# Kernel optimization log

Measured on AMD Instinct MI355X. Metric: run time of the kernel, lower is better.

The kernel has to match this reference:

```python
import jax, jax.numpy as jnp
import numpy as np

N_BOOK = 16  # == len_code; C() loop is only consistent when len_code == n_book


def setup_inputs() -> dict:
    key = jax.random.key(0)
    k1, k2 = jax.random.split(key)
    N = 32768
    D = 256        # len_code * n_book = 16 * 16
    n_classes = 4096
    features = jax.random.normal(k1, (N, D), dtype=jnp.float32)
    # Prototypes passed transposed relative to storage: [len_code*n_book, n_classes]
    Prototypes = jax.random.normal(k2, (D, n_classes), dtype=jnp.float32)
    return {"features": features, "Prototypes": Prototypes}


def reference(features, Prototypes):
    # Faithful to GPQSoftMaxNet.C: per-book matmul, concat over books, mean.
    # features: [N, len_code*n_book] split along dim 1 into chunks of width n_book
    # Prototypes: [len_code*n_book, n_classes] split along dim 0 into chunks of height n_book
    n_book = N_BOOK
    N, D = features.shape
    n_classes = Prototypes.shape[1]
    f = features.reshape(N, -1, n_book)          # [N, n_book(=len_code), n_book]
    P = Prototypes.reshape(-1, n_book, n_classes)  # [n_book(=len_code), n_book, n_classes]
    # mean over books of per-book GEMMs, fused into one einsum (no [N,C,n_book] intermediate)
    logits = jnp.einsum('nbd,bdc->nc', f, P) / jnp.float32(n_book)
    return logits
```

## Files before the change

### kernel.cpp

```cpp
#include <hip/hip_runtime.h>
#include <hip/hip_bf16.h>

typedef __attribute__((ext_vector_type(8))) short short8;
typedef __attribute__((ext_vector_type(4))) float f32x4;

static constexpr int MT = 32768;
static constexpr int KT = 256;
static constexpr int CT = 4096;

__device__ __forceinline__ unsigned short f2b(float f) {
  unsigned int b = __float_as_uint(f);
  b += 0x7FFFu + ((b >> 16) & 1u);
  return (unsigned short)(b >> 16);
}

__global__ void __launch_bounds__(256) cvt_kernel(const float* __restrict__ A,
                                                  const float* __restrict__ B,
                                                  unsigned short* __restrict__ Abf,
                                                  unsigned short* __restrict__ Bt) {
  __shared__ unsigned short tile[32][33];
  int bid = blockIdx.x, tid = threadIdx.x;
  if (bid < 4096) {
    int i = bid * 256 + tid;
    const float4 v0 = reinterpret_cast<const float4*>(A)[2 * i];
    const float4 v1 = reinterpret_cast<const float4*>(A)[2 * i + 1];
    short8 o;
    o[0] = (short)f2b(v0.x); o[1] = (short)f2b(v0.y);
    o[2] = (short)f2b(v0.z); o[3] = (short)f2b(v0.w);
    o[4] = (short)f2b(v1.x); o[5] = (short)f2b(v1.y);
    o[6] = (short)f2b(v1.z); o[7] = (short)f2b(v1.w);
    reinterpret_cast<short8*>(Abf)[i] = o;
  } else {
    int b = bid - 4096;
    int c0 = (b & 127) * 32, k0 = (b >> 7) * 32;
    int tx = tid & 31, ty0 = tid >> 5;
#pragma unroll
    for (int i = 0; i < 4; ++i) {
      int ty = ty0 + i * 8;
      tile[ty][tx] = f2b(B[(size_t)(k0 + ty) * CT + c0 + tx]);
    }
    __syncthreads();
#pragma unroll
    for (int i = 0; i < 4; ++i) {
      int cy = ty0 + i * 8;
      Bt[(size_t)(c0 + cy) * KT + k0 + tx] = tile[tx][cy];
    }
  }
}

__device__ __forceinline__ void gload16(const void* g, void* l) {
  __builtin_amdgcn_global_load_lds(
      (const __attribute__((address_space(1))) void*)g,
      (__attribute__((address_space(3))) void*)l, 16, 0, 0);
}

__global__ void __launch_bounds__(256, 2) gemm_kernel(const unsigned short* __restrict__ Abf,
                                                      const unsigned short* __restrict__ Btw,
                                                      float* __restrict__ O) {
  constexpr int BK = 32;
  __shared__ __align__(16) char smem[32 * 264 * 4];
  unsigned short* Al = (unsigned short*)smem;
  unsigned short* Bl = (unsigned short*)(smem + 8192);
  float* eb = (float*)smem;

  int bid = blockIdx.x;
  int wg = (bid & 7) * 512 + (bid >> 3);
  int tc = wg & 15;
  int tr = wg >> 4;
  int r0 = tr * 128, c0 = tc * 256;

  int tid = threadIdx.x;
  int lane = tid & 63, wid = tid >> 6;
  int wr = wid >> 1, wc = wid & 1;
  int l15 = lane & 15, l4 = lane >> 4;

  f32x4 acc[8][4] = {};

  for (int t = 0; t < KT / BK; ++t) {
    if (t) __syncthreads();
#pragma unroll
    for (int i = 0; i < 2; ++i) {
      int c = wid * 64 + i * 256 + lane;
      gload16(Abf + (size_t)(r0 + (c >> 2)) * KT + t * BK + (c & 3) * 8,
              Al + (wid * 64 + i * 256) * 8);
    }
#pragma unroll
    for (int i = 0; i < 4; ++i) {
      int c = wid * 64 + i * 256 + lane;
      gload16(Btw + (size_t)(c0 + (c >> 2)) * KT + t * BK + (c & 3) * 8,
              Bl + (wid * 64 + i * 256) * 8);
    }
    __syncthreads();

    short8 af[4], bf[8];
#pragma unroll
    for (int m = 0; m < 4; ++m)
      af[m] = *reinterpret_cast<const short8*>(Al + (wr * 64 + m * 16 + l15) * BK + l4 * 8);
#pragma unroll
    for (int n = 0; n < 8; ++n)
      bf[n] = *reinterpret_cast<const short8*>(Bl + (wc * 128 + n * 16 + l15) * BK + l4 * 8);
#pragma unroll
    for (int n = 0; n < 8; ++n)
#pragma unroll
      for (int m = 0; m < 4; ++m)
        acc[n][m] = __builtin_amdgcn_mfma_f32_16x16x32_bf16(bf[n], af[m], acc[n][m], 0, 0, 0);
  }

  const float s = 1.0f / 16.0f;
#pragma unroll
  for (int p = 0; p < 4; ++p) {
    __syncthreads();
    if (wr == (p >> 1)) {
#pragma unroll
      for (int mm = 0; mm < 2; ++mm) {
        int m = (p & 1) * 2 + mm;
#pragma unroll
        for (int n = 0; n < 8; ++n) {
          f32x4 v = acc[n][m];
          v[0] *= s; v[1] *= s; v[2] *= s; v[3] *= s;
          *reinterpret_cast<f32x4*>(
              &eb[(mm * 16 + l15) * 264 + wc * 128 + n * 16 + l4 * 4]) = v;
        }
      }
    }
    __syncthreads();
#pragma unroll
    for (int i = 0; i < 8; ++i) {
      int r = i * 4 + wid;
      f32x4 v = *reinterpret_cast<const f32x4*>(&eb[r * 264 + lane * 4]);
      __builtin_nontemporal_store(v, reinterpret_cast<f32x4*>(
          O + (size_t)(r0 + p * 32 + r) * CT + c0 + lane * 4));
    }
  }
}

__global__ void __launch_bounds__(256) naive_kernel(const float* __restrict__ A,
                                                    const float* __restrict__ B,
                                                    float* __restrict__ O) {
  size_t i = (size_t)blockIdx.x * 256 + threadIdx.x;
  int col = (int)(i & (size_t)(CT - 1));
  int row = (int)(i >> 12);
  float s = 0.f;
  for (int k = 0; k < KT; ++k)
    s += A[(size_t)row * KT + k] * B[(size_t)k * CT + col];
  O[i] = s * (1.0f / 16.0f);
}

extern "C" void kernel_launch(void* const* d_in, const int* in_sizes, int n_in,
                              void* d_out, int out_size, void* d_ws, size_t ws_size,
                              hipStream_t stream) {
  const float* A = (const float*)d_in[0];
  const float* B = (const float*)d_in[1];
  float* O = (float*)d_out;
  const size_t needA = (size_t)MT * KT * sizeof(unsigned short);
  const size_t needB = (size_t)CT * KT * sizeof(unsigned short);
  if (ws_size >= needA + needB) {
    unsigned short* Abf = (unsigned short*)d_ws;
    unsigned short* Btw = (unsigned short*)((char*)d_ws + needA);
    cvt_kernel<<<4096 + 1024, 256, 0, stream>>>(A, B, Abf, Btw);
    gemm_kernel<<<(MT / 128) * (CT / 256), 256, 0, stream>>>(Abf, Btw, O);
  } else {
    naive_kernel<<<(unsigned)((size_t)MT * CT / 256), 256, 0, stream>>>(A, B, O);
  }
}
```

Baseline: 135.9 us.

## Double GEMM K-tile to 64 and XOR-swizzle LDS layout

Raises the K tile from 32 to 64, halving the number of K iterations and their block-wide barriers. Each tile is consumed in two sub-steps of 32. The LDS layout is XOR-swizzled on the 16-byte slot index so that the longer 128-byte rows do not produce bank conflicts on the fragment reads. LDS use grows to 48 KB per block, which may limit how many blocks fit per CU alongside the launch bound of 2.

```diff
diff --git a/kernel.cpp b/kernel.cpp
--- a/kernel.cpp
+++ b/kernel.cpp
@@ -57,10 +57,10 @@
 __global__ void __launch_bounds__(256, 2) gemm_kernel(const unsigned short* __restrict__ Abf,
                                                       const unsigned short* __restrict__ Btw,
                                                       float* __restrict__ O) {
-  constexpr int BK = 32;
-  __shared__ __align__(16) char smem[32 * 264 * 4];
+  constexpr int BK = 64;
+  __shared__ __align__(16) char smem[48 * 1024];
   unsigned short* Al = (unsigned short*)smem;
-  unsigned short* Bl = (unsigned short*)(smem + 8192);
+  unsigned short* Bl = (unsigned short*)(smem + 16384);
   float* eb = (float*)smem;
 
   int bid = blockIdx.x;
@@ -79,31 +79,42 @@
   for (int t = 0; t < KT / BK; ++t) {
     if (t) __syncthreads();
 #pragma unroll
-    for (int i = 0; i < 2; ++i) {
-      int c = wid * 64 + i * 256 + lane;
-      gload16(Abf + (size_t)(r0 + (c >> 2)) * KT + t * BK + (c & 3) * 8,
-              Al + (wid * 64 + i * 256) * 8);
+    for (int i = 0; i < 4; ++i) {
+      int c = i * 256 + wid * 64 + lane;
+      int sc = (c & 7) ^ ((c >> 3) & 7);
+      gload16(Abf + (size_t)(r0 + (c >> 3)) * KT + t * BK + sc * 8,
+              Al + (i * 256 + wid * 64) * 8);
     }
 #pragma unroll
-    for (int i = 0; i < 4; ++i) {
-      int c = wid * 64 + i * 256 + lane;
-      gload16(Btw + (size_t)(c0 + (c >> 2)) * KT + t * BK + (c & 3) * 8,
-              Bl + (wid * 64 + i * 256) * 8);
+    for (int i = 0; i < 8; ++i) {
+      int c = i * 256 + wid * 64 + lane;
+      int sc = (c & 7) ^ ((c >> 3) & 7);
+      gload16(Btw + (size_t)(c0 + (c >> 3)) * KT + t * BK + sc * 8,
+              Bl + (i * 256 + wid * 64) * 8);
     }
     __syncthreads();
 
-    short8 af[4], bf[8];
 #pragma unroll
-    for (int m = 0; m < 4; ++m)
-      af[m] = *reinterpret_cast<const short8*>(Al + (wr * 64 + m * 16 + l15) * BK + l4 * 8);
+    for (int ks = 0; ks < 2; ++ks) {
+      short8 af[4], bf[8];
 #pragma unroll
-    for (int n = 0; n < 8; ++n)
-      bf[n] = *reinterpret_cast<const short8*>(Bl + (wc * 128 + n * 16 + l15) * BK + l4 * 8);
+      for (int m = 0; m < 4; ++m) {
+        int row = wr * 64 + m * 16 + l15;
+        int slot = (ks * 4 + l4) ^ (l15 & 7);
+        af[m] = *reinterpret_cast<const short8*>(Al + row * BK + slot * 8);
+      }
 #pragma unroll
-    for (int n = 0; n < 8; ++n)
+      for (int n = 0; n < 8; ++n) {
+        int row = wc * 128 + n * 16 + l15;
+        int slot = (ks * 4 + l4) ^ (l15 & 7);
+        bf[n] = *reinterpret_cast<const short8*>(Bl + row * BK + slot * 8);
+      }
 #pragma unroll
-      for (int m = 0; m < 4; ++m)
-        acc[n][m] = __builtin_amdgcn_mfma_f32_16x16x32_bf16(bf[n], af[m], acc[n][m], 0, 0, 0);
+      for (int n = 0; n < 8; ++n)
+#pragma unroll
+        for (int m = 0; m < 4; ++m)
+          acc[n][m] = __builtin_amdgcn_mfma_f32_16x16x32_bf16(bf[n], af[m], acc[n][m], 0, 0, 0);
+    }
   }
 
   const float s = 1.0f / 16.0f;
```

Result: faster. 125.9 us (-7.4%).
